# Kernel optimization log

Measured on AMD Instinct MI355X. Metric: run time of the kernel, lower is better.

## Reference

```python
import jax, jax.numpy as jnp
import numpy as np

TAU = 1.0
EPS_MASS = 1e-6
EPS_LOG = 1e-8
EPS_DEN = 1e-8


def setup_inputs() -> dict:
    key = jax.random.key(0)
    k1, k2, k3, k4 = jax.random.split(key, 4)
    B, T, P, D, R, K = 4, 1024, 16, 64, 32, 64
    m = jax.random.normal(k1, (B, T, P, D), dtype=jnp.float32)
    w = jax.random.uniform(k2, (B, T, P), dtype=jnp.float32)
    p = jax.random.uniform(k3, (B, T, P, K), dtype=jnp.float32)
    patch_centers = jax.random.normal(k4, (R, D), dtype=jnp.float32)
    return {"m": m, "w": w, "p": p, "patch_centers": patch_centers}


def reference(m, w, p, patch_centers):
    # m: [B,T,P,D], w: [B,T,P], p: [B,T,P,K], patch_centers: [R,D]
    R = patch_centers.shape[0]
    # squared distances patch-component -> center: [B,T,P,R]
    diff = m[..., None, :] - patch_centers  # [B,T,P,R,D]
    dists = jnp.sum(diff * diff, axis=-1)
    gamma = jax.nn.softmax(-dists / TAU, axis=-1)  # [B,T,P,R]
    start_mass = gamma * w[..., None]  # [B,T,P,R]
    total_mass_r = start_mass.sum(axis=2)  # [B,T,R]
    p_bar_num = jnp.einsum('btpk,btpr->btrk', p, start_mass)  # [B,T,R,K]
    p_bar = p_bar_num / (total_mass_r[..., None] + EPS_MASS)
    # pairwise center affinity omega: [R,R]
    cdiff = patch_centers[:, None, :] - patch_centers[None, :, :]
    center_dists = jnp.sum(cdiff * cdiff, axis=-1)
    omega = jnp.exp(-center_dists / TAU)
    # pairwise JS divergence over K: [B,T,R,R]
    p_r = p_bar[:, :, :, None, :]  # [B,T,R,1,K]
    p_s = p_bar[:, :, None, :, :]  # [B,T,1,R,K]
    m_dist = 0.5 * (p_r + p_s)
    log_m = jnp.log(m_dist + EPS_LOG)
    kl_r = jnp.sum(p_r * (jnp.log(p_r + EPS_LOG) - log_m), axis=-1)
    kl_s = jnp.sum(p_s * (jnp.log(p_s + EPS_LOG) - log_m), axis=-1)
    js_rs = 0.5 * (kl_r + kl_s)  # [B,T,R,R]
    weighted_js = omega * js_rs
    mask = jnp.triu(jnp.ones((R, R), dtype=jnp.float32), k=1)
    loss = jnp.sum(weighted_js * mask) / (jnp.sum(mask) + EPS_DEN)
    return loss
```

## Files before the change

kernel.cpp:

```cpp
#include <hip/hip_runtime.h>

#define PP 16
#define DD 64
#define RR 32
#define KK 64
#define NBT 4096

#define LOG2E 1.4426950408889634f
#define LN2   0.6931471805599453f
#define D2_CUT 25.0f

static __device__ __forceinline__ float fast_log2(float x) { return __builtin_amdgcn_logf(x); }
static __device__ __forceinline__ float fast_exp2(float x) { return __builtin_amdgcn_exp2f(x); }
static __device__ __forceinline__ float fast_rcp(float x)  { return __builtin_amdgcn_rcpf(x); }

__global__ __launch_bounds__(1024) void prune_kernel(const float* __restrict__ c,
                                                     float* __restrict__ cc,
                                                     int* __restrict__ npairs,
                                                     float2* __restrict__ plist) {
    __shared__ float red[16];
    __shared__ float dmin_sh;
    __shared__ int cnt;
    const int t = threadIdx.x;
    const int r = t >> 5, s = t & 31;
    const bool active = s > r;

    float d2 = 0.f;
#pragma unroll 8
    for (int d = 0; d < DD; ++d) {
        float diff = c[r * DD + d] - c[s * DD + d];
        d2 = fmaf(diff, diff, d2);
    }
    float dm = active ? d2 : 3.4e38f;
#pragma unroll
    for (int off = 32; off > 0; off >>= 1) dm = fminf(dm, __shfl_down(dm, off, 64));
    if ((t & 63) == 0) red[t >> 6] = dm;
    if (t == 0) cnt = 0;
    __syncthreads();
    if (t < 64) {
        float v = (t < 16) ? red[t] : 3.4e38f;
#pragma unroll
        for (int off = 8; off > 0; off >>= 1) v = fminf(v, __shfl_down(v, off, 64));
        if (t == 0) dmin_sh = v;
    }
    __syncthreads();
    const float dmin = dmin_sh;
    if (active && d2 <= dmin + D2_CUT) {
        int idx = atomicAdd(&cnt, 1);
        plist[idx] = make_float2(fast_exp2(-d2 * LOG2E), __int_as_float(t));
    }
    if (t < RR) {
        float a2 = 0.f;
#pragma unroll 8
        for (int d = 0; d < DD; ++d) { float v = c[t * DD + d]; a2 = fmaf(v, v, a2); }
        cc[t] = a2;
    }
    __syncthreads();
    if (t == 0) *npairs = cnt;
}

__global__ __launch_bounds__(256) void sheaf2_kernel(
    const float* __restrict__ m, const float* __restrict__ w,
    const float* __restrict__ p, const float* __restrict__ c,
    const float* __restrict__ cc, const int* __restrict__ npairs,
    const float2* __restrict__ plist, float* __restrict__ partials) {
    __shared__ float2 sm_cT2[32 * 33];
    __shared__ float  sm_mass[PP * 36];
    __shared__ __align__(16) float2 sm_pl[RR * KK];
    __shared__ float  sm_sw[PP];
    __shared__ float  sred[4];

    const int tid = threadIdx.x;
    const int bt  = blockIdx.x;

    {
        const float2* c2 = (const float2*)c;
#pragma unroll
        for (int it = 0; it < 4; ++it) {
            int idx = tid + 256 * it;
            int rr = idx >> 5, d2i = idx & 31;
            sm_cT2[d2i * 33 + rr] = c2[idx];
        }
    }
    __syncthreads();

    {
        const int r  = tid & 31;
        const int pg = tid >> 5;
        const float4* m4a = (const float4*)(m + ((size_t)bt * PP + pg) * DD);
        const float4* m4b = m4a + (8 * DD) / 4;
        float ccr = cc[r];
        float acc0 = 0.f, acc1 = 0.f;
#pragma unroll
        for (int d4 = 0; d4 < 16; ++d4) {
            float2 ca = sm_cT2[(2 * d4) * 33 + r];
            float2 cb = sm_cT2[(2 * d4 + 1) * 33 + r];
            float4 ma = m4a[d4];
            float4 mb = m4b[d4];
            acc0 = fmaf(ma.x, ca.x, acc0); acc0 = fmaf(ma.y, ca.y, acc0);
            acc0 = fmaf(ma.z, cb.x, acc0); acc0 = fmaf(ma.w, cb.y, acc0);
            acc1 = fmaf(mb.x, ca.x, acc1); acc1 = fmaf(mb.y, ca.y, acc1);
            acc1 = fmaf(mb.z, cb.x, acc1); acc1 = fmaf(mb.w, cb.y, acc1);
        }
        sm_mass[pg * 36 + r]       = fmaf(2.f, acc0, -ccr);
        sm_mass[(pg + 8) * 36 + r] = fmaf(2.f, acc1, -ccr);
    }
    __syncthreads();

    if (tid < PP) {
        float4* row4 = (float4*)&sm_mass[tid * 36];
        float4 v[8];
        float mx = -3.4e38f;
#pragma unroll
        for (int i = 0; i < 8; ++i) {
            v[i] = row4[i];
            mx = fmaxf(mx, fmaxf(fmaxf(v[i].x, v[i].y), fmaxf(v[i].z, v[i].w)));
        }
        float ssum = 0.f;
#pragma unroll
        for (int i = 0; i < 8; ++i) {
            v[i].x = fast_exp2((v[i].x - mx) * LOG2E);
            v[i].y = fast_exp2((v[i].y - mx) * LOG2E);
            v[i].z = fast_exp2((v[i].z - mx) * LOG2E);
            v[i].w = fast_exp2((v[i].w - mx) * LOG2E);
            ssum += (v[i].x + v[i].y) + (v[i].z + v[i].w);
            row4[i] = v[i];
        }
        sm_sw[tid] = w[(size_t)bt * PP + tid] * fast_rcp(ssum);
    }
    __syncthreads();

    if (tid < RR) {
        float ef[PP];
        float tot = 0.f;
#pragma unroll
        for (int pi = 0; pi < PP; ++pi) {
            ef[pi] = sm_mass[pi * 36 + tid] * sm_sw[pi];
            tot += ef[pi];
        }
        float inv = fast_rcp(tot + 1e-6f);
#pragma unroll
        for (int pi = 0; pi < PP; ++pi) sm_mass[pi * 36 + tid] = ef[pi] * inv;
    }
    __syncthreads();

    {
        const int k  = tid & 63;
        const int wv = tid >> 6;
        const int r0 = wv * 8;
        const float* pg_ = p + (size_t)bt * PP * KK + k;
        float pcol[PP];
#pragma unroll
        for (int pi = 0; pi < PP; ++pi) pcol[pi] = pg_[pi * KK];
        float acc[8] = {0.f, 0.f, 0.f, 0.f, 0.f, 0.f, 0.f, 0.f};
#pragma unroll
        for (int pi = 0; pi < PP; ++pi) {
            float4 ma = *(const float4*)&sm_mass[pi * 36 + r0];
            float4 mb = *(const float4*)&sm_mass[pi * 36 + r0 + 4];
            acc[0] = fmaf(pcol[pi], ma.x, acc[0]);
            acc[1] = fmaf(pcol[pi], ma.y, acc[1]);
            acc[2] = fmaf(pcol[pi], ma.z, acc[2]);
            acc[3] = fmaf(pcol[pi], ma.w, acc[3]);
            acc[4] = fmaf(pcol[pi], mb.x, acc[4]);
            acc[5] = fmaf(pcol[pi], mb.y, acc[5]);
            acc[6] = fmaf(pcol[pi], mb.z, acc[6]);
            acc[7] = fmaf(pcol[pi], mb.w, acc[7]);
        }
#pragma unroll
        for (int j = 0; j < 8; ++j) {
            float pb = acc[j];
            float l2 = fast_log2(pb + 1e-8f);
            sm_pl[(r0 + j) * KK + k] = make_float2(pb, pb * l2);
        }
    }
    __syncthreads();

    {
        const int k  = tid & 63;
        const int wv = __builtin_amdgcn_readfirstlane(tid >> 6);
        const int np = __builtin_amdgcn_readfirstlane(*npairs);
        float acc = 0.f;
        for (int i = wv; i < np; i += 4) {
            float2 e = plist[i];
            int rs = __float_as_int(e.y);
            int r = rs >> 5, s = rs & 31;
            float2 a = sm_pl[r * KK + k];
            float2 b = sm_pl[s * KK + k];
            float sum = a.x + b.x;
            float t   = a.y + b.y;
            float lm  = fast_log2(fmaf(0.5f, sum, 1e-8f));
            t = fmaf(-sum, lm, t);
            acc = fmaf(e.x, t, acc);
        }
#pragma unroll
        for (int off = 32; off > 0; off >>= 1) acc += __shfl_down(acc, off, 64);
        if (k == 0) sred[tid >> 6] = acc;
    }
    __syncthreads();
    if (tid == 0) {
        float tot = (sred[0] + sred[1]) + (sred[2] + sred[3]);
        partials[bt] = tot * (0.5f * LN2 / 496.0f);
    }
}

__global__ __launch_bounds__(256) void reduce_kernel(const float* __restrict__ partials,
                                                     float* __restrict__ out) {
    __shared__ float sred[4];
    const int tid = threadIdx.x;
    const float4* p4 = (const float4*)partials;
    float acc = 0.f;
#pragma unroll
    for (int i = 0; i < 4; ++i) {
        float4 v = p4[tid + 256 * i];
        acc += (v.x + v.y) + (v.z + v.w);
    }
#pragma unroll
    for (int off = 32; off > 0; off >>= 1) acc += __shfl_down(acc, off, 64);
    if ((tid & 63) == 0) sred[tid >> 6] = acc;
    __syncthreads();
    if (tid == 0) out[0] = (sred[0] + sred[1]) + (sred[2] + sred[3]);
}

extern "C" void kernel_launch(void* const* d_in, const int* in_sizes, int n_in,
                              void* d_out, int out_size, void* d_ws, size_t ws_size,
                              hipStream_t stream) {
    const float* m = (const float*)d_in[0];
    const float* w = (const float*)d_in[1];
    const float* p = (const float*)d_in[2];
    const float* c = (const float*)d_in[3];
    float* out = (float*)d_out;

    float* wsf      = (float*)d_ws;
    int*   npairs   = (int*)d_ws;
    float* cc       = wsf + 64;
    float2* plist   = (float2*)(wsf + 128);
    float* partials = wsf + 2048;

    prune_kernel<<<1, 1024, 0, stream>>>(c, cc, npairs, plist);
    sheaf2_kernel<<<NBT, 256, 0, stream>>>(m, w, p, c, cc, npairs, plist, partials);
    reduce_kernel<<<1, 256, 0, stream>>>(partials, out);
}
```

Measured before the change: 110.5 us.

## Fuse final reduction into main kernel, stage inputs in LDS, parallelize softmax

Folds the separate reduce kernel into the main kernel using a last-block atomic counter, removing one launch. Stages m, p and the pair list in shared memory with coalesced float4 loads, and aliases buffers to keep LDS usage bounded. Softmax and mass normalization now run across 64 threads using cross-lane shuffles instead of 16 and 32 serial threads, merging two barriers. The prune kernel is vectorized with float4 loads. The change adds an atomic and fence per block and increases shared-memory footprint.

```diff
diff --git a/kernel.cpp b/kernel.cpp
--- a/kernel.cpp
+++ b/kernel.cpp
@@ -9,6 +9,7 @@
 #define LOG2E 1.4426950408889634f
 #define LN2   0.6931471805599453f
 #define D2_CUT 25.0f
+#define MAXPAIRS 496
 
 static __device__ __forceinline__ float fast_log2(float x) { return __builtin_amdgcn_logf(x); }
 static __device__ __forceinline__ float fast_exp2(float x) { return __builtin_amdgcn_exp2f(x); }
@@ -16,7 +17,7 @@
 
 __global__ __launch_bounds__(1024) void prune_kernel(const float* __restrict__ c,
                                                      float* __restrict__ cc,
-                                                     int* __restrict__ npairs,
+                                                     int* __restrict__ meta,
                                                      float2* __restrict__ plist) {
     __shared__ float red[16];
     __shared__ float dmin_sh;
@@ -24,18 +25,22 @@
     const int t = threadIdx.x;
     const int r = t >> 5, s = t & 31;
     const bool active = s > r;
+    const float4* c4 = (const float4*)c;
 
     float d2 = 0.f;
-#pragma unroll 8
-    for (int d = 0; d < DD; ++d) {
-        float diff = c[r * DD + d] - c[s * DD + d];
-        d2 = fmaf(diff, diff, d2);
-    }
+#pragma unroll
+    for (int d4 = 0; d4 < 16; ++d4) {
+        float4 a = c4[r * 16 + d4];
+        float4 b = c4[s * 16 + d4];
+        float dx = a.x - b.x, dy = a.y - b.y, dz = a.z - b.z, dw = a.w - b.w;
+        d2 = fmaf(dx, dx, d2); d2 = fmaf(dy, dy, d2);
+        d2 = fmaf(dz, dz, d2); d2 = fmaf(dw, dw, d2);
+    }
+    if (t == 0) cnt = 0;
     float dm = active ? d2 : 3.4e38f;
 #pragma unroll
     for (int off = 32; off > 0; off >>= 1) dm = fminf(dm, __shfl_down(dm, off, 64));
     if ((t & 63) == 0) red[t >> 6] = dm;
-    if (t == 0) cnt = 0;
     __syncthreads();
     if (t < 64) {
         float v = (t < 16) ? red[t] : 3.4e38f;
@@ -44,59 +49,75 @@
         if (t == 0) dmin_sh = v;
     }
     __syncthreads();
-    const float dmin = dmin_sh;
-    if (active && d2 <= dmin + D2_CUT) {
+    if (active && d2 <= dmin_sh + D2_CUT) {
         int idx = atomicAdd(&cnt, 1);
         plist[idx] = make_float2(fast_exp2(-d2 * LOG2E), __int_as_float(t));
     }
     if (t < RR) {
         float a2 = 0.f;
-#pragma unroll 8
-        for (int d = 0; d < DD; ++d) { float v = c[t * DD + d]; a2 = fmaf(v, v, a2); }
+#pragma unroll
+        for (int d4 = 0; d4 < 16; ++d4) {
+            float4 v = c4[t * 16 + d4];
+            a2 = fmaf(v.x, v.x, a2); a2 = fmaf(v.y, v.y, a2);
+            a2 = fmaf(v.z, v.z, a2); a2 = fmaf(v.w, v.w, a2);
+        }
         cc[t] = a2;
     }
     __syncthreads();
-    if (t == 0) *npairs = cnt;
+    if (t == 0) { meta[0] = cnt; meta[1] = 0; }
 }
 
 __global__ __launch_bounds__(256) void sheaf2_kernel(
     const float* __restrict__ m, const float* __restrict__ w,
     const float* __restrict__ p, const float* __restrict__ c,
-    const float* __restrict__ cc, const int* __restrict__ npairs,
-    const float2* __restrict__ plist, float* __restrict__ partials) {
-    __shared__ float2 sm_cT2[32 * 33];
-    __shared__ float  sm_mass[PP * 36];
-    __shared__ __align__(16) float2 sm_pl[RR * KK];
-    __shared__ float  sm_sw[PP];
-    __shared__ float  sred[4];
+    const float* __restrict__ cc, const int* __restrict__ meta,
+    const float2* __restrict__ plist, float* __restrict__ partials,
+    float* __restrict__ out) {
+    __shared__ __align__(16) float  smem_mp[PP * DD];
+    __shared__ __align__(16) float  sm_p[PP * KK];
+    __shared__ __align__(16) float2 smem_cpl[RR * KK];
+    __shared__ float sm_mass[PP * 36];
+    __shared__ float sm_w[PP];
+    __shared__ float sred[4];
+    __shared__ int   sm_last;
+
+    float*  sm_m     = smem_mp;
+    float2* sm_plist = (float2*)smem_mp;
+    float2* sm_cT2   = smem_cpl;
+    float2* sm_pl    = smem_cpl;
 
     const int tid = threadIdx.x;
     const int bt  = blockIdx.x;
-
-    {
+    const int k   = tid & 63;
+    const int wv  = tid >> 6;
+    const int np  = meta[0];
+
+    {
+        const float4* m4 = (const float4*)(m + (size_t)bt * PP * DD);
+        const float4* p4 = (const float4*)(p + (size_t)bt * PP * KK);
+        ((float4*)sm_m)[tid] = m4[tid];
+        ((float4*)sm_p)[tid] = p4[tid];
         const float2* c2 = (const float2*)c;
 #pragma unroll
         for (int it = 0; it < 4; ++it) {
             int idx = tid + 256 * it;
-            int rr = idx >> 5, d2i = idx & 31;
-            sm_cT2[d2i * 33 + rr] = c2[idx];
-        }
+            sm_cT2[(idx & 31) * 33 + (idx >> 5)] = c2[idx];
+        }
+        if (tid < PP) sm_w[tid] = w[(size_t)bt * PP + tid];
     }
     __syncthreads();
 
     {
         const int r  = tid & 31;
         const int pg = tid >> 5;
-        const float4* m4a = (const float4*)(m + ((size_t)bt * PP + pg) * DD);
-        const float4* m4b = m4a + (8 * DD) / 4;
         float ccr = cc[r];
         float acc0 = 0.f, acc1 = 0.f;
 #pragma unroll
         for (int d4 = 0; d4 < 16; ++d4) {
             float2 ca = sm_cT2[(2 * d4) * 33 + r];
             float2 cb = sm_cT2[(2 * d4 + 1) * 33 + r];
-            float4 ma = m4a[d4];
-            float4 mb = m4b[d4];
+            float4 ma = *(const float4*)&sm_m[pg * DD + d4 * 4];
+            float4 mb = *(const float4*)&sm_m[(pg + 8) * DD + d4 * 4];
             acc0 = fmaf(ma.x, ca.x, acc0); acc0 = fmaf(ma.y, ca.y, acc0);
             acc0 = fmaf(ma.z, cb.x, acc0); acc0 = fmaf(ma.w, cb.y, acc0);
             acc1 = fmaf(mb.x, ca.x, acc1); acc1 = fmaf(mb.y, ca.y, acc1);
@@ -107,64 +128,58 @@
     }
     __syncthreads();
 
-    if (tid < PP) {
-        float4* row4 = (float4*)&sm_mass[tid * 36];
-        float4 v[8];
-        float mx = -3.4e38f;
-#pragma unroll
-        for (int i = 0; i < 8; ++i) {
-            v[i] = row4[i];
-            mx = fmaxf(mx, fmaxf(fmaxf(v[i].x, v[i].y), fmaxf(v[i].z, v[i].w)));
-        }
+    if (tid < 64) {
+        const int pidx = tid & 15;
+        const int rc   = tid >> 4;
+        float* row = &sm_mass[pidx * 36 + rc * 8];
+        float4 va = *(float4*)row;
+        float4 vb = *(float4*)(row + 4);
+        float v[8] = {va.x, va.y, va.z, va.w, vb.x, vb.y, vb.z, vb.w};
+        float mx = v[0];
+#pragma unroll
+        for (int j = 1; j < 8; ++j) mx = fmaxf(mx, v[j]);
+        mx = fmaxf(mx, __shfl_xor(mx, 16, 64));
+        mx = fmaxf(mx, __shfl_xor(mx, 32, 64));
         float ssum = 0.f;
 #pragma unroll
-        for (int i = 0; i < 8; ++i) {
-            v[i].x = fast_exp2((v[i].x - mx) * LOG2E);
-            v[i].y = fast_exp2((v[i].y - mx) * LOG2E);
-            v[i].z = fast_exp2((v[i].z - mx) * LOG2E);
-            v[i].w = fast_exp2((v[i].w - mx) * LOG2E);
-            ssum += (v[i].x + v[i].y) + (v[i].z + v[i].w);
-            row4[i] = v[i];
-        }
-        sm_sw[tid] = w[(size_t)bt * PP + tid] * fast_rcp(ssum);
-    }
-    __syncthreads();
-
-    if (tid < RR) {
-        float ef[PP];
-        float tot = 0.f;
+        for (int j = 0; j < 8; ++j) { v[j] = fast_exp2((v[j] - mx) * LOG2E); ssum += v[j]; }
+        ssum += __shfl_xor(ssum, 16, 64);
+        ssum += __shfl_xor(ssum, 32, 64);
+        float sw = sm_w[pidx] * fast_rcp(ssum);
+#pragma unroll
+        for (int j = 0; j < 8; ++j) v[j] *= sw;
+#pragma unroll
+        for (int j = 0; j < 8; ++j) {
+            float tj = v[j];
+            tj += __shfl_xor(tj, 1, 64);
+            tj += __shfl_xor(tj, 2, 64);
+            tj += __shfl_xor(tj, 4, 64);
+            tj += __shfl_xor(tj, 8, 64);
+            v[j] *= fast_rcp(tj + 1e-6f);
+        }
+        *(float4*)row       = make_float4(v[0], v[1], v[2], v[3]);
+        *(float4*)(row + 4) = make_float4(v[4], v[5], v[6], v[7]);
+    } else {
+        for (int i = tid - 64; i < np; i += 192) sm_plist[i] = plist[i];
+    }
+    __syncthreads();
+
+    {
+        const int r0 = wv * 8;
+        float acc[8] = {0.f, 0.f, 0.f, 0.f, 0.f, 0.f, 0.f, 0.f};
 #pragma unroll
         for (int pi = 0; pi < PP; ++pi) {
-            ef[pi] = sm_mass[pi * 36 + tid] * sm_sw[pi];
-            tot += ef[pi];
-        }
-        float inv = fast_rcp(tot + 1e-6f);
-#pragma unroll
-        for (int pi = 0; pi < PP; ++pi) sm_mass[pi * 36 + tid] = ef[pi] * inv;
-    }
-    __syncthreads();
-
-    {
-        const int k  = tid & 63;
-        const int wv = tid >> 6;
-        const int r0 = wv * 8;
-        const float* pg_ = p + (size_t)bt * PP * KK + k;
-        float pcol[PP];
-#pragma unroll
-        for (int pi = 0; pi < PP; ++pi) pcol[pi] = pg_[pi * KK];
-        float acc[8] = {0.f, 0.f, 0.f, 0.f, 0.f, 0.f, 0.f, 0.f};
-#pragma unroll
-        for (int pi = 0; pi < PP; ++pi) {
+            float pv = sm_p[pi * KK + k];
             float4 ma = *(const float4*)&sm_mass[pi * 36 + r0];
             float4 mb = *(const float4*)&sm_mass[pi * 36 + r0 + 4];
-            acc[0] = fmaf(pcol[pi], ma.x, acc[0]);
-            acc[1] = fmaf(pcol[pi], ma.y, acc[1]);
-            acc[2] = fmaf(pcol[pi], ma.z, acc[2]);
-            acc[3] = fmaf(pcol[pi], ma.w, acc[3]);
-            acc[4] = fmaf(pcol[pi], mb.x, acc[4]);
-            acc[5] = fmaf(pcol[pi], mb.y, acc[5]);
-            acc[6] = fmaf(pcol[pi], mb.z, acc[6]);
-            acc[7] = fmaf(pcol[pi], mb.w, acc[7]);
+            acc[0] = fmaf(pv, ma.x, acc[0]);
+            acc[1] = fmaf(pv, ma.y, acc[1]);
+            acc[2] = fmaf(pv, ma.z, acc[2]);
+            acc[3] = fmaf(pv, ma.w, acc[3]);
+            acc[4] = fmaf(pv, mb.x, acc[4]);
+            acc[5] = fmaf(pv, mb.y, acc[5]);
+            acc[6] = fmaf(pv, mb.z, acc[6]);
+            acc[7] = fmaf(pv, mb.w, acc[7]);
         }
 #pragma unroll
         for (int j = 0; j < 8; ++j) {
@@ -176,12 +191,9 @@
     __syncthreads();
 
     {
-        const int k  = tid & 63;
-        const int wv = __builtin_amdgcn_readfirstlane(tid >> 6);
-        const int np = __builtin_amdgcn_readfirstlane(*npairs);
         float acc = 0.f;
         for (int i = wv; i < np; i += 4) {
-            float2 e = plist[i];
+            float2 e = sm_plist[i];
             int rs = __float_as_int(e.y);
             int r = rs >> 5, s = rs & 31;
             float2 a = sm_pl[r * KK + k];
@@ -194,31 +206,34 @@
         }
 #pragma unroll
         for (int off = 32; off > 0; off >>= 1) acc += __shfl_down(acc, off, 64);
-        if (k == 0) sred[tid >> 6] = acc;
-    }
-    __syncthreads();
+        if (k == 0) sred[wv] = acc;
+    }
+    __syncthreads();
+
+    int* done = (int*)&(((int*)meta)[1]);
     if (tid == 0) {
         float tot = (sred[0] + sred[1]) + (sred[2] + sred[3]);
         partials[bt] = tot * (0.5f * LN2 / 496.0f);
-    }
-}
-
-__global__ __launch_bounds__(256) void reduce_kernel(const float* __restrict__ partials,
-                                                     float* __restrict__ out) {
-    __shared__ float sred[4];
-    const int tid = threadIdx.x;
-    const float4* p4 = (const float4*)partials;
-    float acc = 0.f;
-#pragma unroll
-    for (int i = 0; i < 4; ++i) {
-        float4 v = p4[tid + 256 * i];
-        acc += (v.x + v.y) + (v.z + v.w);
-    }
-#pragma unroll
-    for (int off = 32; off > 0; off >>= 1) acc += __shfl_down(acc, off, 64);
-    if ((tid & 63) == 0) sred[tid >> 6] = acc;
-    __syncthreads();
-    if (tid == 0) out[0] = (sred[0] + sred[1]) + (sred[2] + sred[3]);
+        __threadfence();
+        int old = atomicAdd(done, 1);
+        sm_last = (old == NBT - 1) ? 1 : 0;
+    }
+    __syncthreads();
+    if (sm_last) {
+        __threadfence();
+        const float4* p4 = (const float4*)partials;
+        float acc = 0.f;
+#pragma unroll
+        for (int i = 0; i < 4; ++i) {
+            float4 v = p4[tid + 256 * i];
+            acc += (v.x + v.y) + (v.z + v.w);
+        }
+#pragma unroll
+        for (int off = 32; off > 0; off >>= 1) acc += __shfl_down(acc, off, 64);
+        if (k == 0) sred[wv] = acc;
+        __syncthreads();
+        if (tid == 0) out[0] = (sred[0] + sred[1]) + (sred[2] + sred[3]);
+    }
 }
 
 extern "C" void kernel_launch(void* const* d_in, const int* in_sizes, int n_in,
@@ -231,12 +246,11 @@
     float* out = (float*)d_out;
 
     float* wsf      = (float*)d_ws;
-    int*   npairs   = (int*)d_ws;
+    int*   meta     = (int*)d_ws;
     float* cc       = wsf + 64;
     float2* plist   = (float2*)(wsf + 128);
     float* partials = wsf + 2048;
 
-    prune_kernel<<<1, 1024, 0, stream>>>(c, cc, npairs, plist);
-    sheaf2_kernel<<<NBT, 256, 0, stream>>>(m, w, p, c, cc, npairs, plist, partials);
-    reduce_kernel<<<1, 256, 0, stream>>>(partials, out);
+    prune_kernel<<<1, 1024, 0, stream>>>(c, cc, meta, plist);
+    sheaf2_kernel<<<NBT, 256, 0, stream>>>(m, w, p, c, cc, meta, plist, partials, out);
 }
```

Measured after the change: 179.1 us. 62.1% more time.
